# Optimization experiments

Hardware: AMD Instinct MI355X
Metric: run time of the kernel (lower is better)

Reference implementation:

```python
import jax, jax.numpy as jnp
import numpy as np

EPS = 1e-7  # Keras K.epsilon()


def setup_inputs() -> dict:
    key = jax.random.key(0)
    k_x, k_w, k_b, k_u = jax.random.split(key, 4)
    B, T, D, A = 256, 512, 256, 50
    x = jax.random.normal(k_x, (B, T, D), dtype=jnp.float32)
    # Keras initializers.get('normal') -> stddev 0.05 RandomNormal
    W = jax.random.normal(k_w, (D, A), dtype=jnp.float32) * 0.05
    b = jax.random.normal(k_b, (A,), dtype=jnp.float32) * 0.05
    u = jax.random.normal(k_u, (A, 1), dtype=jnp.float32) * 0.05
    return {"x": x, "W": W, "b": b, "u": u}


def reference(x, W, b, u):
    # uit: [B, T, A]
    uit = jnp.tanh(jnp.einsum('btd,da->bta', x, W) + b)
    # ait: [B, T] raw scores -> exp-normalize (as in original, no max-subtract)
    ait = jnp.einsum('bta,a->bt', uit, u[:, 0])
    ait = jnp.exp(ait)
    ait = ait / (jnp.sum(ait, axis=1, keepdims=True) + EPS)
    # weighted pool over time: [B, D]
    return jnp.einsum('btd,bt->bd', x, ait)
```

## Files before the change

### kernel.cpp

```cpp
#include <hip/hip_runtime.h>
#include <math.h>

#define B_  256
#define T_  512
#define D_  256
#define A_  50
#define AP  52
#define APL 53
#define EPS 1e-7f

__global__ void pad_w_kernel(const float* __restrict__ W, float* __restrict__ Wp)
{
    int idx = blockIdx.x * 256 + threadIdx.x;
    if (idx >= D_ * AP) return;
    int d = idx / AP;
    int a = idx - d * AP;
    Wp[idx] = (a < A_) ? W[d * A_ + a] : 0.0f;
}

__global__ __launch_bounds__(512)
void scores_kernel(const float* __restrict__ x, const float* __restrict__ Wp,
                   const float* __restrict__ bias, const float* __restrict__ u,
                   float* __restrict__ s_out, float* __restrict__ partial)
{
    __shared__ float accL[256 * APL];
    __shared__ float red[256];

    const int tid = threadIdx.x;
    const int h   = __builtin_amdgcn_readfirstlane(tid >> 8);
    const int rl  = tid & 255;
    const size_t r = (size_t)blockIdx.x * 256 + rl;

    const float4* __restrict__ xr4 = (const float4*)(x + r * D_) + h * 32;
    const float*  __restrict__ Wh  = Wp + (size_t)h * 128 * AP;

    float acc[AP];
    #pragma unroll
    for (int a = 0; a < AP; a++) acc[a] = 0.0f;

    for (int d4 = 0; d4 < 32; d4++) {
        const float4 xv = xr4[d4];
        const float xr[4] = {xv.x, xv.y, xv.z, xv.w};
        #pragma unroll
        for (int j = 0; j < 4; j++) {
            const float4* __restrict__ wrow =
                (const float4*)(Wh + (size_t)(d4 * 4 + j) * AP);
            #pragma unroll
            for (int a4 = 0; a4 < AP / 4; a4++) {
                const float4 w = wrow[a4];
                acc[4 * a4 + 0] += xr[j] * w.x;
                acc[4 * a4 + 1] += xr[j] * w.y;
                acc[4 * a4 + 2] += xr[j] * w.z;
                acc[4 * a4 + 3] += xr[j] * w.w;
            }
        }
    }

    if (h == 1) {
        #pragma unroll
        for (int a = 0; a < AP; a++) accL[rl * APL + a] = acc[a];
    }
    __syncthreads();

    if (h == 0) {
        float sc = 0.0f;
        #pragma unroll
        for (int a = 0; a < A_; a++) {
            float v = acc[a] + accL[rl * APL + a] + bias[a];
            sc += tanhf(v) * u[a];
        }
        const float s = expf(sc);
        s_out[r] = s;
        red[rl] = s;
    }
    __syncthreads();

    for (int off = 128; off > 0; off >>= 1) {
        if (tid < off) red[tid] += red[tid + off];
        __syncthreads();
    }
    if (tid == 0) partial[blockIdx.x] = red[0];
}

__global__ __launch_bounds__(256)
void pool_kernel(const float* __restrict__ x, const float* __restrict__ s_in,
                 const float* __restrict__ partial, float* __restrict__ pp)
{
    __shared__ float s_lds[64];
    __shared__ float part[4 * 256];

    const int tid = threadIdx.x;
    const int bb  = blockIdx.x >> 3;
    const int q   = blockIdx.x & 7;

    const float inv = 1.0f / (partial[2 * bb] + partial[2 * bb + 1] + EPS);
    if (tid < 64)
        s_lds[tid] = s_in[(size_t)bb * T_ + q * 64 + tid] * inv;
    __syncthreads();

    const int w = tid >> 6;
    const int l = tid & 63;

    const float* __restrict__ xb = x + ((size_t)bb * T_ + q * 64) * D_;
    float4 acc = make_float4(0.f, 0.f, 0.f, 0.f);

    #pragma unroll
    for (int i = 0; i < 16; i++) {
        const int t = w * 16 + i;
        float4 xv = *(const float4*)(xb + (size_t)t * D_ + l * 4);
        float sv  = s_lds[t];
        acc.x += xv.x * sv;
        acc.y += xv.y * sv;
        acc.z += xv.z * sv;
        acc.w += xv.w * sv;
    }

    part[w * 256 + l * 4 + 0] = acc.x;
    part[w * 256 + l * 4 + 1] = acc.y;
    part[w * 256 + l * 4 + 2] = acc.z;
    part[w * 256 + l * 4 + 3] = acc.w;
    __syncthreads();

    pp[(size_t)blockIdx.x * 256 + tid] =
        part[tid] + part[256 + tid] + part[512 + tid] + part[768 + tid];
}

__global__ __launch_bounds__(256)
void combine_kernel(const float* __restrict__ pp, float* __restrict__ out)
{
    const size_t idx = (size_t)blockIdx.x * 256 + threadIdx.x;
    const size_t b   = idx >> 8;
    const size_t d   = idx & 255;
    float o = 0.0f;
    #pragma unroll
    for (int q = 0; q < 8; q++) o += pp[(b * 8 + q) * 256 + d];
    out[idx] = o;
}

extern "C" void kernel_launch(void* const* d_in, const int* in_sizes, int n_in,
                              void* d_out, int out_size, void* d_ws, size_t ws_size,
                              hipStream_t stream)
{
    const float* x = (const float*)d_in[0];
    const float* W = (const float*)d_in[1];
    const float* b = (const float*)d_in[2];
    const float* u = (const float*)d_in[3];

    float* scores  = (float*)d_ws;
    float* partial = scores + (size_t)B_ * T_;
    float* Wp      = partial + 512;
    float* pp      = Wp + (size_t)D_ * AP;
    float* out     = (float*)d_out;

    pad_w_kernel   <<<(D_ * AP + 255) / 256, 256, 0, stream>>>(W, Wp);
    scores_kernel  <<<(B_ * T_) / 256, 512, 0, stream>>>(x, Wp, b, u, scores, partial);
    pool_kernel    <<<B_ * 8, 256, 0, stream>>>(x, scores, partial, pp);
    combine_kernel <<<B_, 256, 0, stream>>>(pp, out);
}
```

Baseline: 257.8 us.

## Compute attention scores with bf16 MFMA instead of scalar FP32 FMAs

Replaces the per-row scalar FP32 projection x·W with 16x16x32 bf16 MFMA instructions. W is pre-swizzled into the MFMA B-operand layout, and x is converted to bf16 on the fly. The tanh/u reduction now uses cross-lane shuffles within 16-lane groups, and the block-level sum reduction uses a single thread over 64 values. It removes the large LDS accumulator exchange and the FP32 ALU-bound inner loop. In exchange, bf16 rounding of x and W reduces score precision before the exp, and the pool kernel's normalisation is adapted to 8 partial sums per batch row.

```diff
diff --git a/kernel.cpp b/kernel.cpp
--- a/kernel.cpp
+++ b/kernel.cpp
@@ -5,81 +5,111 @@
 #define T_  512
 #define D_  256
 #define A_  50
-#define AP  52
-#define APL 53
 #define EPS 1e-7f
 
-__global__ void pad_w_kernel(const float* __restrict__ W, float* __restrict__ Wp)
+typedef short  short8  __attribute__((ext_vector_type(8)));
+typedef float  floatx4 __attribute__((ext_vector_type(4)));
+
+__device__ inline unsigned short f2bf(float f) {
+    unsigned int u = __float_as_uint(f);
+    u = (u + 0x7fffu + ((u >> 16) & 1u)) >> 16;
+    return (unsigned short)u;
+}
+
+__global__ void prep_kernel(const float* __restrict__ W,
+                            const float* __restrict__ bias,
+                            const float* __restrict__ u,
+                            unsigned short* __restrict__ Wf,
+                            float* __restrict__ bu64)
 {
     int idx = blockIdx.x * 256 + threadIdx.x;
-    if (idx >= D_ * AP) return;
-    int d = idx / AP;
-    int a = idx - d * AP;
-    Wp[idx] = (a < A_) ? W[d * A_ + a] : 0.0f;
+    int j  = idx & 7;
+    int l  = (idx >> 3) & 63;
+    int ks = (idx >> 9) & 7;
+    int nt = idx >> 12;
+    int n  = nt * 16 + (l & 15);
+    int k  = ks * 32 + (l >> 4) * 8 + j;
+    float val = (n < A_) ? W[k * A_ + n] : 0.0f;
+    Wf[idx] = f2bf(val);
+    if (idx < 64) {
+        bu64[idx]      = (idx < A_) ? bias[idx] : 0.0f;
+        bu64[64 + idx] = (idx < A_) ? u[idx]    : 0.0f;
+    }
 }
 
-__global__ __launch_bounds__(512)
-void scores_kernel(const float* __restrict__ x, const float* __restrict__ Wp,
-                   const float* __restrict__ bias, const float* __restrict__ u,
+__global__ __launch_bounds__(256)
+void scores_kernel(const float* __restrict__ x,
+                   const unsigned short* __restrict__ Wf,
+                   const float* __restrict__ bu64,
                    float* __restrict__ s_out, float* __restrict__ partial)
 {
-    __shared__ float accL[256 * APL];
-    __shared__ float red[256];
+    __shared__ float sred[64];
 
-    const int tid = threadIdx.x;
-    const int h   = __builtin_amdgcn_readfirstlane(tid >> 8);
-    const int rl  = tid & 255;
-    const size_t r = (size_t)blockIdx.x * 256 + rl;
+    const int tid  = threadIdx.x;
+    const int w    = tid >> 6;
+    const int l    = tid & 63;
+    const int c    = l & 15;
+    const int quad = l >> 4;
+    const size_t rowbase = (size_t)blockIdx.x * 64 + w * 16;
 
-    const float4* __restrict__ xr4 = (const float4*)(x + r * D_) + h * 32;
-    const float*  __restrict__ Wh  = Wp + (size_t)h * 128 * AP;
+    const float4* __restrict__ xrow = (const float4*)(x + (rowbase + c) * D_);
+    const short8* __restrict__ wf8  = (const short8*)Wf;
 
-    float acc[AP];
+    float bnc[4], unc[4];
     #pragma unroll
-    for (int a = 0; a < AP; a++) acc[a] = 0.0f;
+    for (int nt = 0; nt < 4; nt++) {
+        bnc[nt] = bu64[nt * 16 + c];
+        unc[nt] = bu64[64 + nt * 16 + c];
+    }
 
-    for (int d4 = 0; d4 < 32; d4++) {
-        const float4 xv = xr4[d4];
-        const float xr[4] = {xv.x, xv.y, xv.z, xv.w};
+    floatx4 acc[4];
+    #pragma unroll
+    for (int nt = 0; nt < 4; nt++) acc[nt] = (floatx4){0.f, 0.f, 0.f, 0.f};
+
+    #pragma unroll
+    for (int ks = 0; ks < 8; ks++) {
+        const float4 a0 = xrow[ks * 8 + quad * 2];
+        const float4 a1 = xrow[ks * 8 + quad * 2 + 1];
+        short8 av;
+        av[0] = (short)f2bf(a0.x); av[1] = (short)f2bf(a0.y);
+        av[2] = (short)f2bf(a0.z); av[3] = (short)f2bf(a0.w);
+        av[4] = (short)f2bf(a1.x); av[5] = (short)f2bf(a1.y);
+        av[6] = (short)f2bf(a1.z); av[7] = (short)f2bf(a1.w);
         #pragma unroll
-        for (int j = 0; j < 4; j++) {
-            const float4* __restrict__ wrow =
-                (const float4*)(Wh + (size_t)(d4 * 4 + j) * AP);
-            #pragma unroll
-            for (int a4 = 0; a4 < AP / 4; a4++) {
-                const float4 w = wrow[a4];
-                acc[4 * a4 + 0] += xr[j] * w.x;
-                acc[4 * a4 + 1] += xr[j] * w.y;
-                acc[4 * a4 + 2] += xr[j] * w.z;
-                acc[4 * a4 + 3] += xr[j] * w.w;
-            }
+        for (int nt = 0; nt < 4; nt++) {
+            const short8 bv = wf8[(nt * 8 + ks) * 64 + l];
+            acc[nt] = __builtin_amdgcn_mfma_f32_16x16x32_bf16(av, bv, acc[nt], 0, 0, 0);
         }
     }
 
-    if (h == 1) {
+    float part[4];
+    #pragma unroll
+    for (int r = 0; r < 4; r++) {
+        float v = 0.0f;
         #pragma unroll
-        for (int a = 0; a < AP; a++) accL[rl * APL + a] = acc[a];
+        for (int nt = 0; nt < 4; nt++)
+            v += tanhf(acc[nt][r] + bnc[nt]) * unc[nt];
+        #pragma unroll
+        for (int off = 1; off < 16; off <<= 1)
+            v += __shfl_xor(v, off, 16);
+        part[r] = v;
+    }
+
+    if (c == 0) {
+        #pragma unroll
+        for (int r = 0; r < 4; r++) {
+            const float s = expf(part[r]);
+            s_out[rowbase + quad * 4 + r] = s;
+            sred[w * 16 + quad * 4 + r] = s;
+        }
     }
     __syncthreads();
-
-    if (h == 0) {
-        float sc = 0.0f;
+    if (tid == 0) {
+        float s = 0.0f;
         #pragma unroll
-        for (int a = 0; a < A_; a++) {
-            float v = acc[a] + accL[rl * APL + a] + bias[a];
-            sc += tanhf(v) * u[a];
-        }
-        const float s = expf(sc);
-        s_out[r] = s;
-        red[rl] = s;
+        for (int i = 0; i < 64; i++) s += sred[i];
+        partial[blockIdx.x] = s;
     }
-    __syncthreads();
-
-    for (int off = 128; off > 0; off >>= 1) {
-        if (tid < off) red[tid] += red[tid + off];
-        __syncthreads();
-    }
-    if (tid == 0) partial[blockIdx.x] = red[0];
 }
 
 __global__ __launch_bounds__(256)
@@ -93,7 +123,11 @@
     const int bb  = blockIdx.x >> 3;
     const int q   = blockIdx.x & 7;
 
-    const float inv = 1.0f / (partial[2 * bb] + partial[2 * bb + 1] + EPS);
+    float den = EPS;
+    #pragma unroll
+    for (int i = 0; i < 8; i++) den += partial[bb * 8 + i];
+    const float inv = 1.0f / den;
+
     if (tid < 64)
         s_lds[tid] = s_in[(size_t)bb * T_ + q * 64 + tid] * inv;
     __syncthreads();
@@ -148,12 +182,13 @@
 
     float* scores  = (float*)d_ws;
     float* partial = scores + (size_t)B_ * T_;
-    float* Wp      = partial + 512;
-    float* pp      = Wp + (size_t)D_ * AP;
+    float* bu64    = partial + 2048;
+    float* pp      = bu64 + 128;
+    unsigned short* Wf = (unsigned short*)(pp + (size_t)B_ * 8 * 256);
     float* out     = (float*)d_out;
 
-    pad_w_kernel   <<<(D_ * AP + 255) / 256, 256, 0, stream>>>(W, Wp);
-    scores_kernel  <<<(B_ * T_) / 256, 512, 0, stream>>>(x, Wp, b, u, scores, partial);
-    pool_kernel    <<<B_ * 8, 256, 0, stream>>>(x, scores, partial, pp);
-    combine_kernel <<<B_, 256, 0, stream>>>(pp, out);
+    prep_kernel   <<<64,   256, 0, stream>>>(W, b, u, Wf, bu64);
+    scores_kernel <<<2048, 256, 0, stream>>>(x, Wf, bu64, scores, partial);
+    pool_kernel   <<<2048, 256, 0, stream>>>(x, scores, partial, pp);
+    combine_kernel<<<B_,   256, 0, stream>>>(pp, out);
 }
```

Result: faster. 224.4 us (-13.0%).
